# Kernel optimization log

Hardware: AMD Instinct MI355X
Metric: run time of the kernel (lower is better)

The kernel has to match this reference:

```python
import jax, jax.numpy as jnp
import numpy as np

B, S, HID = 4, 8192, 768
H, D, K = 12, 64, 16
KW = 4
TTT_BASE_LR = 1.0
ROPE_THETA = 10000.0
ETA_DECAY_RATE = 0.0
LN_EPS = 1e-5


def setup_inputs() -> dict:
    key = jax.random.key(0)
    ks = jax.random.split(key, 12)
    def randn(k, shape, scale):
        return jax.random.normal(k, shape, jnp.float32) * scale
    def lecun(k, fan_in, shape):
        return jax.random.normal(k, shape, jnp.float32) / np.sqrt(fan_in).astype(np.float32)
    return {
        "x": randn(ks[0], (B, S, HID), 1.0),
        "wq": lecun(ks[1], HID, (HID, H * D)),
        "wv": lecun(ks[2], HID, (HID, H * D)),
        "wo": lecun(ks[3], H * D, (H * D, HID)),  # zeros in source init; randomized for a non-trivial baseline
        "wg": lecun(ks[4], HID, (HID, H * D)),
        "conv_q_w": randn(ks[5], (KW, H * D), 0.1),
        "conv_q_b": jnp.zeros((H * D,), jnp.float32),
        "conv_k_w": randn(ks[6], (KW, H * D), 0.1),
        "conv_k_b": jnp.zeros((H * D,), jnp.float32),
        "lr_w": randn(ks[7], (H, HID), 0.02),
        "lr_b": jnp.zeros((H,), jnp.float32),
        "learnable_token_idx": jnp.zeros((K,), jnp.float32),
        "ttt_norm_scale": jnp.ones((H, 1, D), jnp.float32),
        "ttt_norm_bias": jnp.zeros((H, 1, D), jnp.float32),
        "post_norm_scale": jnp.ones((H * D,), jnp.float32),
        "post_norm_bias": jnp.zeros((H * D,), jnp.float32),
        "W1": randn(ks[8], (H, D, D), 0.02),
        "b1": jnp.zeros((H, 1, D), jnp.float32),
    }


def causal_dwconv(x, w, b):
    # x: [B,S,C], w: [KW,C], b: [C]. Replicates left-pad(KW-1) + flax SAME conv + crop:
    # out[t] = b + sum_k w[k] * x[t + k - KW]  (strictly causal, excludes current token)
    S_ = x.shape[1]
    xp = jnp.pad(x, ((0, 0), (KW, 0), (0, 0)))
    out = b
    for k in range(KW):
        out = out + w[k] * xp[:, k:k + S_]
    return out


def rope(x, cos, sin):
    # x: [B,S,H,D]; interleaved-pair rotation; cos/sin: [S, D//2]
    xr = x.reshape(*x.shape[:-1], D // 2, 2)
    x1, x2 = xr[..., 0], xr[..., 1]
    c = cos[None, :, None, :]
    s = sin[None, :, None, :]
    return jnp.stack([x1 * c - x2 * s, x1 * s + x2 * c], axis=-1).reshape(x.shape)


def ln_fwd(x, g, b):
    mu = x.mean(-1, keepdims=True)
    var = x.var(-1, keepdims=True)
    return (x - mu) * jax.lax.rsqrt(var + LN_EPS) * g + b


def ln_l2_bwd(x, target, g, b):
    # grad of 0.5*||LN(x)*g+b - target||^2 wrt x (fused form)
    mu = x.mean(-1, keepdims=True)
    var = x.var(-1, keepdims=True)
    std = jnp.sqrt(var + LN_EPS)
    xh = (x - mu) / std
    gx = (xh * g + b - target) * g
    return (gx - gx.mean(-1, keepdims=True) - xh * (gx * xh).mean(-1, keepdims=True)) / std


def ttt_forward(x, wq, wv, wo, wg, conv_q_w, conv_q_b, conv_k_w, conv_k_b,
                lr_w, lr_b, learnable_token_idx, ttt_norm_scale, ttt_norm_bias,
                post_norm_scale, post_norm_bias, W1, b1):
    Bx, Sx, _ = x.shape
    n_mb = Sx // K
    xqk = x @ wq
    XQ = causal_dwconv(xqk, conv_q_w, conv_q_b).reshape(Bx, Sx, H, D)
    XK = causal_dwconv(xqk, conv_k_w, conv_k_b).reshape(Bx, Sx, H, D)
    XV = (x @ wv).reshape(Bx, Sx, H, D)

    inv_freq = 1.0 / (ROPE_THETA ** (jnp.arange(0, D, 2, dtype=jnp.float32) / D))
    freqs = jnp.arange(Sx, dtype=jnp.float32)[:, None] * inv_freq[None, :]
    cos, sin = jnp.cos(freqs), jnp.sin(freqs)
    XQ = rope(XQ, cos, sin)
    XK = rope(XK, cos, sin)

    # per-token learning rates
    token_idx = jnp.maximum(1.0 / jnp.arange(1, K + 1, dtype=jnp.float32) + learnable_token_idx, 0.0)  # [K]
    ttt_lr = jax.nn.sigmoid(jnp.einsum('bsd,hd->bhs', x, lr_w) + lr_b[None, :, None])  # [B,H,S]
    ttt_lr_eta = (TTT_BASE_LR / D) * ttt_lr
    decay = jnp.exp(ETA_DECAY_RATE * (jnp.arange(K, dtype=jnp.float32) - (K - 1)))  # [K]
    # eta[b,h,m,i,j] = token_idx[i] * lr[b,h,m,j] * decay[j]
    eta = token_idx[None, None, None, :, None] * (ttt_lr_eta.reshape(Bx, H, n_mb, 1, K) * decay)

    to_mb = lambda t: t.reshape(Bx, n_mb, K, H, D).transpose(1, 0, 3, 2, 4)  # [n_mb,B,H,K,D]
    xs = (to_mb(XQ), to_mb(XK), to_mb(XV), eta.transpose(2, 0, 1, 3, 4))

    W1_0 = jnp.broadcast_to(W1[None], (Bx, H, D, D)) + 0.0
    b1_0 = jnp.broadcast_to(b1[None], (Bx, H, 1, D)) + 0.0
    tril = jnp.tril(jnp.ones((K, K), jnp.float32))

    def step(carry, inp):
        W1c, b1c = carry
        q, k, v, e = inp  # [B,H,K,D], e: [B,H,K,K]
        Z1 = jnp.einsum('bhkd,bhde->bhke', k, W1c) + b1c
        grad = ln_l2_bwd(Z1, v - k, ttt_norm_scale, ttt_norm_bias)  # [B,H,K,D]
        Attn = jnp.einsum('bhid,bhjd->bhij', q, k) * tril
        b1_bar = b1c - jnp.einsum('bhij,bhjd->bhid', e * tril, grad)
        Z1_bar = jnp.einsum('bhkd,bhde->bhke', q, W1c) \
                 - jnp.einsum('bhij,bhjd->bhid', e * Attn, grad) + b1_bar
        last_e = e[..., -1, :, None]  # [B,H,K,1]
        W1n = W1c - jnp.einsum('bhkd,bhke->bhde', last_e * k, grad)
        b1n = b1c - jnp.sum(last_e * grad, axis=-2, keepdims=True)
        out = q + ln_fwd(Z1_bar, ttt_norm_scale, ttt_norm_bias)
        return (W1n, b1n), out

    _, Z = jax.lax.scan(step, (W1_0, b1_0), xs)  # Z: [n_mb,B,H,K,D]
    Z = Z.transpose(1, 0, 3, 2, 4).reshape(Bx, Sx, H * D)

    mu = Z.mean(-1, keepdims=True)
    var = Z.var(-1, keepdims=True)
    Zn = (Z - mu) * jax.lax.rsqrt(var + LN_EPS) * post_norm_scale + post_norm_bias
    gate = jax.nn.gelu(x @ wg)
    return (Zn * gate) @ wo


def reference(x, wq, wv, wo, wg, conv_q_w, conv_q_b, conv_k_w, conv_k_b,
              lr_w, lr_b, learnable_token_idx, ttt_norm_scale, ttt_norm_bias,
              post_norm_scale, post_norm_bias, W1, b1):
    return ttt_forward(x, wq, wv, wo, wg, conv_q_w, conv_q_b, conv_k_w, conv_k_b,
                       lr_w, lr_b, learnable_token_idx, ttt_norm_scale, ttt_norm_bias,
                       post_norm_scale, post_norm_bias, W1, b1)
```

## Files before the change

### kernel.cpp

```cpp
#include <hip/hip_runtime.h>
#include <hip/hip_bf16.h>
#include <math.h>

#define BB 4
#define SSEQ 8192
#define HIDDEN 768
#define NH 12
#define DDIM 64
#define KMB 16
#define NMB 512
#define NTOK ((size_t)BB * SSEQ)
#define NELT (NTOK * HIDDEN)
#define WELT (768 * 768)

typedef short bf16x8 __attribute__((ext_vector_type(8)));
typedef float f32x4 __attribute__((ext_vector_type(4)));

union frag_u {
  bf16x8 v;
  unsigned u32[4];
  unsigned short u16[8];
};

__device__ __forceinline__ f32x4 mfma16(bf16x8 a, bf16x8 b, f32x4 c) {
  return __builtin_amdgcn_mfma_f32_16x16x32_bf16(a, b, c, 0, 0, 0);
}

__device__ __forceinline__ float wave_sum(float v) {
#pragma unroll
  for (int off = 32; off > 0; off >>= 1) v += __shfl_xor(v, off, 64);
  return v;
}

template <int CTRL>
__device__ __forceinline__ float dpp_add(float v) {
  union { float f; int i; } a, b;
  a.f = v;
  b.i = __builtin_amdgcn_update_dpp(0, a.i, CTRL, 0xF, 0xF, true);
  return v + b.f;
}
__device__ __forceinline__ float rsum16(float v) {
  v = dpp_add<0x121>(v);
  v = dpp_add<0x122>(v);
  v = dpp_add<0x124>(v);
  v = dpp_add<0x128>(v);
  return v;
}

__device__ __forceinline__ unsigned short bf16hi(float x) {
  union { float f; unsigned u; } a; a.f = x;
  return (unsigned short)((a.u + 0x8000u) >> 16);
}
__device__ __forceinline__ unsigned pack_bf16(float f0, float f1) {
  union { float f; unsigned u; } a, b; a.f = f0; b.f = f1;
  return __builtin_amdgcn_perm(b.u + 0x8000u, a.u + 0x8000u, 0x07060302u);
}
__device__ __forceinline__ float bf2f(unsigned short s) {
  union { unsigned u; float f; } a; a.u = ((unsigned)s) << 16; return a.f;
}
__device__ __forceinline__ float gelu_tanh(float x) {
  float x3 = x * x * x;
  return 0.5f * x * (1.0f + tanhf(0.7978845608028654f * (x + 0.044715f * x3)));
}

__device__ __forceinline__ void glds16(const void* g, void* l) {
  __builtin_amdgcn_global_load_lds(
      (const __attribute__((address_space(1))) void*)g,
      (__attribute__((address_space(3))) void*)l, 16, 0, 0);
}

__global__ __launch_bounds__(256) void cvt_x_kernel(
    const float* __restrict__ x, unsigned short* __restrict__ xb) {
  const size_t gid = (size_t)blockIdx.x * 256 + threadIdx.x;
  const float4 v = *(const float4*)(x + gid * 4);
  uint2 r; r.x = pack_bf16(v.x, v.y); r.y = pack_bf16(v.z, v.w);
  *(uint2*)(xb + gid * 4) = r;
}

__global__ __launch_bounds__(256) void cvt_wT_kernel(
    const float* __restrict__ W, unsigned short* __restrict__ WT) {
  __shared__ float tile[32][33];
  const int tx = threadIdx.x & 31, ty = threadIdx.x >> 5;
  const int k0 = blockIdx.x * 32, n0 = blockIdx.y * 32;
#pragma unroll
  for (int r = 0; r < 4; ++r)
    tile[ty + 8 * r][tx] = W[(size_t)(k0 + ty + 8 * r) * 768 + n0 + tx];
  __syncthreads();
#pragma unroll
  for (int r = 0; r < 4; ++r)
    WT[(size_t)(n0 + ty + 8 * r) * 768 + k0 + tx] = bf16hi(tile[tx][ty + 8 * r]);
}

__global__ __launch_bounds__(256) void gemm_mfma(
    const unsigned short* __restrict__ A, const unsigned short* __restrict__ BT,
    void* __restrict__ Cout, int mode) {
  __shared__ __align__(16) unsigned short Asl[128 * 32];
  __shared__ __align__(16) unsigned short Bsl[128 * 32];
  const int tid = threadIdx.x;
  const int wave = tid >> 6, lane = tid & 63;
  const int n16 = lane & 15, g16 = lane >> 4;
  const int wm = (wave >> 1) * 64, wn = (wave & 1) * 64;
  const int m0 = blockIdx.x * 128, n0 = blockIdx.y * 128;

  const int srow = tid >> 2;
  const int sseg = (tid & 3) * 8;

  const unsigned short* aSrc0 = A + (size_t)(m0 + srow) * 768 + sseg;
  const unsigned short* aSrc1 = A + (size_t)(m0 + 64 + srow) * 768 + sseg;
  const unsigned short* bSrc0 = BT + (size_t)(n0 + srow) * 768 + sseg;
  const unsigned short* bSrc1 = BT + (size_t)(n0 + 64 + srow) * 768 + sseg;
  char* aDst0 = (char*)Asl + wave * 1024;
  char* aDst1 = (char*)Asl + 4096 + wave * 1024;
  char* bDst0 = (char*)Bsl + wave * 1024;
  char* bDst1 = (char*)Bsl + 4096 + wave * 1024;

  f32x4 acc[4][4];
#pragma unroll
  for (int i = 0; i < 4; ++i)
#pragma unroll
    for (int j = 0; j < 4; ++j) { acc[i][j][0] = 0.f; acc[i][j][1] = 0.f; acc[i][j][2] = 0.f; acc[i][j][3] = 0.f; }

  for (int k0 = 0; k0 < 768; k0 += 32) {
    __syncthreads();
    glds16(aSrc0 + k0, aDst0);
    glds16(aSrc1 + k0, aDst1);
    glds16(bSrc0 + k0, bDst0);
    glds16(bSrc1 + k0, bDst1);
    __syncthreads();
    bf16x8 af[4], bfr[4];
#pragma unroll
    for (int mf = 0; mf < 4; ++mf)
      af[mf] = *(const bf16x8*)(Asl + (wm + mf * 16 + n16) * 32 + g16 * 8);
#pragma unroll
    for (int nf = 0; nf < 4; ++nf)
      bfr[nf] = *(const bf16x8*)(Bsl + (wn + nf * 16 + n16) * 32 + g16 * 8);
#pragma unroll
    for (int mf = 0; mf < 4; ++mf)
#pragma unroll
      for (int nf = 0; nf < 4; ++nf)
        acc[mf][nf] = mfma16(af[mf], bfr[nf], acc[mf][nf]);
  }

  const int erow0 = m0 + wm + 4 * g16;
  const int ecol0 = n0 + wn + n16;
  if (mode == 2) {
    float* C = (float*)Cout;
#pragma unroll
    for (int mf = 0; mf < 4; ++mf)
#pragma unroll
      for (int nf = 0; nf < 4; ++nf)
#pragma unroll
        for (int r = 0; r < 4; ++r)
          C[(size_t)(erow0 + mf * 16 + r) * HIDDEN + ecol0 + nf * 16] = acc[mf][nf][r];
  } else if (mode == 1) {
    unsigned short* C = (unsigned short*)Cout;
#pragma unroll
    for (int mf = 0; mf < 4; ++mf)
#pragma unroll
      for (int nf = 0; nf < 4; ++nf)
#pragma unroll
        for (int r = 0; r < 4; ++r)
          C[(size_t)(erow0 + mf * 16 + r) * HIDDEN + ecol0 + nf * 16] = bf16hi(gelu_tanh(acc[mf][nf][r]));
  } else {
    unsigned short* C = (unsigned short*)Cout;
#pragma unroll
    for (int mf = 0; mf < 4; ++mf)
#pragma unroll
      for (int nf = 0; nf < 4; ++nf)
#pragma unroll
        for (int r = 0; r < 4; ++r)
          C[(size_t)(erow0 + mf * 16 + r) * HIDDEN + ecol0 + nf * 16] = bf16hi(acc[mf][nf][r]);
  }
}

__global__ __launch_bounds__(256) void lrpre_kernel(
    const float* __restrict__ x, const float* __restrict__ lrw,
    const float* __restrict__ lrb, float* __restrict__ lrpre) {
  const int g = threadIdx.x >> 6, l = threadIdx.x & 63;
  const int t = blockIdx.x * 4 + g;
  const float* xr = x + (size_t)t * HIDDEN;
  float xv[12];
#pragma unroll
  for (int j = 0; j < 12; ++j) xv[j] = xr[l + 64 * j];
  const int b = t >> 13, s = t & (SSEQ - 1);
  for (int h = 0; h < NH; ++h) {
    const float* wr = lrw + (size_t)h * HIDDEN;
    float a = 0.f;
#pragma unroll
    for (int j = 0; j < 12; ++j) a += xv[j] * wr[l + 64 * j];
    a = wave_sum(a);
    if (l == 0) lrpre[((size_t)b * NH + h) * SSEQ + s] = a + lrb[h];
  }
}

__global__ __launch_bounds__(256) void convrope_kernel(
    const __hip_bfloat16* __restrict__ xqk,
    const float* __restrict__ cqw, const float* __restrict__ cqb,
    const float* __restrict__ ckw, const float* __restrict__ ckb,
    __hip_bfloat16* __restrict__ XQ, __hip_bfloat16* __restrict__ XK) {
  const size_t gid = (size_t)blockIdx.x * 256 + threadIdx.x;
  const int p = (int)(gid % 384);
  const size_t bt = gid / 384;
  const int t = (int)(bt & (SSEQ - 1));
  const int c0 = 2 * p, c1 = c0 + 1;
  float q0 = cqb[c0], q1 = cqb[c1], k0v = ckb[c0], k1v = ckb[c1];
#pragma unroll
  for (int kk = 0; kk < 4; ++kk) {
    const int tp = t - 4 + kk;
    if (tp >= 0) {
      const size_t src = (bt - t + tp) * HIDDEN;
      const float x0 = __bfloat162float(xqk[src + c0]);
      const float x1 = __bfloat162float(xqk[src + c1]);
      q0  += cqw[kk * HIDDEN + c0] * x0;  q1  += cqw[kk * HIDDEN + c1] * x1;
      k0v += ckw[kk * HIDDEN + c0] * x0;  k1v += ckw[kk * HIDDEN + c1] * x1;
    }
  }
  const int f = p & 31;
  const float invf = expf(-(float)f * 0.28782313662425572f);
  const float ang = (float)t * invf;
  float sn, cs;
  sincosf(ang, &sn, &cs);
  const size_t o = bt * HIDDEN;
  XQ[o + c0] = __float2bfloat16(q0 * cs - q1 * sn);
  XQ[o + c1] = __float2bfloat16(q0 * sn + q1 * cs);
  XK[o + c0] = __float2bfloat16(k0v * cs - k1v * sn);
  XK[o + c1] = __float2bfloat16(k0v * sn + k1v * cs);
}

struct ScanBuf {
  uint2 qa[2][2], ka[2][2], va[2][2];
  float lr[4];
};

__global__ __launch_bounds__(64) void scan_mfma_kernel(
    const __hip_bfloat16* __restrict__ XQg, const __hip_bfloat16* __restrict__ XKg,
    const __hip_bfloat16* __restrict__ XVg, const float* __restrict__ lrpre,
    const float* __restrict__ lti, const float* __restrict__ tnsg,
    const float* __restrict__ tnbg, const float* __restrict__ W1g,
    const float* __restrict__ b1g, __hip_bfloat16* __restrict__ Zg) {
  const int bh = blockIdx.x;
  const int b = bh / NH, h = bh % NH;
  const int lane = threadIdx.x;
  const int n = lane & 15, g16 = lane >> 4;
  const float inv64 = 1.0f / 64.0f;

  const unsigned short* XQb = (const unsigned short*)XQg + (size_t)b * SSEQ * HIDDEN + h * 64;
  const unsigned short* XKb = (const unsigned short*)XKg + (size_t)b * SSEQ * HIDDEN + h * 64;
  const unsigned short* XVb = (const unsigned short*)XVg + (size_t)b * SSEQ * HIDDEN + h * 64;
  unsigned short* Zb = (unsigned short*)Zg + (size_t)b * SSEQ * HIDDEN + h * 64;
  const float* lrp = lrpre + ((size_t)b * NH + h) * SSEQ;

  f32x4 W1acc[4][4];
#pragma unroll
  for (int db = 0; db < 4; ++db)
#pragma unroll
    for (int eb = 0; eb < 4; ++eb)
#pragma unroll
      for (int r = 0; r < 4; ++r)
        W1acc[db][eb][r] = W1g[(size_t)h * 4096 + (16 * db + 4 * g16 + r) * 64 + 16 * eb + n];

  float b1r[4], tnsr[4], tnbr[4];
#pragma unroll
  for (int eb = 0; eb < 4; ++eb) {
    const int e = h * 64 + 16 * eb + n;
    b1r[eb] = b1g[e]; tnsr[eb] = tnsg[e]; tnbr[eb] = tnbg[e];
  }
  const float tok_n = fmaxf(1.0f / (float)(n + 1) + lti[n], 0.0f);
  const float tok15 = __shfl(tok_n, 15, 64);

  frag_u id0, id1;
  {
    const unsigned short onebf = (g16 == (n >> 2)) ? (unsigned short)0x3F80 : (unsigned short)0;
    const unsigned vsh = ((unsigned)onebf) << (16 * (n & 1));
    const unsigned lo = ((n & 2) == 0) ? vsh : 0u;
    const unsigned hi = ((n & 2) != 0) ? vsh : 0u;
    id0.u32[0] = lo; id0.u32[1] = hi; id0.u32[2] = 0; id0.u32[3] = 0;
    id1.u32[0] = 0;  id1.u32[1] = 0;  id1.u32[2] = lo; id1.u32[3] = hi;
  }
  frag_u onesA;
  onesA.u32[0] = 0x3F803F80u; onesA.u32[1] = 0x3F803F80u;
  onesA.u32[2] = 0x3F803F80u; onesA.u32[3] = 0x3F803F80u;

  int offA[2][2], offC[4][4];
#pragma unroll
  for (int c = 0; c < 2; ++c)
#pragma unroll
    for (int jg = 0; jg < 2; ++jg)
      offA[c][jg] = n * HIDDEN + 16 * (2 * c + jg) + 4 * g16;
#pragma unroll
  for (int blk = 0; blk < 4; ++blk)
#pragma unroll
    for (int r = 0; r < 4; ++r)
      offC[blk][r] = (4 * g16 + r) * HIDDEN + 16 * blk + n;

  auto load_mb = [&](ScanBuf& bf, int mb) {
    const size_t sb = (size_t)mb * (KMB * HIDDEN);
#pragma unroll
    for (int c = 0; c < 2; ++c)
#pragma unroll
      for (int jg = 0; jg < 2; ++jg) {
        bf.qa[c][jg] = *(const uint2*)(XQb + sb + offA[c][jg]);
        bf.ka[c][jg] = *(const uint2*)(XKb + sb + offA[c][jg]);
        bf.va[c][jg] = *(const uint2*)(XVb + sb + offA[c][jg]);
      }
    const float4 l4 = *(const float4*)(lrp + mb * KMB + 4 * g16);
    bf.lr[0] = l4.x; bf.lr[1] = l4.y; bf.lr[2] = l4.z; bf.lr[3] = l4.w;
  };

  auto compute_mb = [&](ScanBuf& bf, int mb) {
    const size_t sb = (size_t)mb * (KMB * HIDDEN);
    float etaj[4];
#pragma unroll
    for (int jj = 0; jj < 4; ++jj)
      etaj[jj] = 1.0f / (64.0f * (1.0f + __expf(-bf.lr[jj])));

    frag_u w1f[2][4];
#pragma unroll
    for (int c = 0; c < 2; ++c)
#pragma unroll
      for (int eb = 0; eb < 4; ++eb) {
        w1f[c][eb].u32[0] = pack_bf16(W1acc[2 * c][eb][0], W1acc[2 * c][eb][1]);
        w1f[c][eb].u32[1] = pack_bf16(W1acc[2 * c][eb][2], W1acc[2 * c][eb][3]);
        w1f[c][eb].u32[2] = pack_bf16(W1acc[2 * c + 1][eb][0], W1acc[2 * c + 1][eb][1]);
        w1f[c][eb].u32[3] = pack_bf16(W1acc[2 * c + 1][eb][2], W1acc[2 * c + 1][eb][3]);
      }
    frag_u kaf[2], qaf[2], vaf[2];
#pragma unroll
    for (int c = 0; c < 2; ++c) {
      kaf[c].u32[0] = bf.ka[c][0].x; kaf[c].u32[1] = bf.ka[c][0].y;
      kaf[c].u32[2] = bf.ka[c][1].x; kaf[c].u32[3] = bf.ka[c][1].y;
      qaf[c].u32[0] = bf.qa[c][0].x; qaf[c].u32[1] = bf.qa[c][0].y;
      qaf[c].u32[2] = bf.qa[c][1].x; qaf[c].u32[3] = bf.qa[c][1].y;
      vaf[c].u32[0] = bf.va[c][0].x; vaf[c].u32[1] = bf.va[c][0].y;
      vaf[c].u32[2] = bf.va[c][1].x; vaf[c].u32[3] = bf.va[c][1].y;
    }

    f32x4 z4; z4[0] = 0.f; z4[1] = 0.f; z4[2] = 0.f; z4[3] = 0.f;
    f32x4 qcf[4], kcf[4], vcf[4];
#pragma unroll
    for (int c = 0; c < 2; ++c) {
      qcf[2 * c]     = mfma16(qaf[c].v, id0.v, z4);
      qcf[2 * c + 1] = mfma16(qaf[c].v, id1.v, z4);
      kcf[2 * c]     = mfma16(kaf[c].v, id0.v, z4);
      kcf[2 * c + 1] = mfma16(kaf[c].v, id1.v, z4);
      vcf[2 * c]     = mfma16(vaf[c].v, id0.v, z4);
      vcf[2 * c + 1] = mfma16(vaf[c].v, id1.v, z4);
    }
    frag_u ktf[4];
#pragma unroll
    for (int mk = 0; mk < 4; ++mk) {
      ktf[mk].u32[0] = pack_bf16(kcf[mk][0], kcf[mk][1]);
      ktf[mk].u32[1] = pack_bf16(kcf[mk][2], kcf[mk][3]);
      ktf[mk].u32[2] = 0; ktf[mk].u32[3] = 0;
    }

    f32x4 zk[4], zq[4];
#pragma unroll
    for (int eb = 0; eb < 4; ++eb) {
      f32x4 init; init[0] = b1r[eb]; init[1] = b1r[eb]; init[2] = b1r[eb]; init[3] = b1r[eb];
      zk[eb] = init; zq[eb] = init;
    }
#pragma unroll
    for (int c = 0; c < 2; ++c)
#pragma unroll
      for (int eb = 0; eb < 4; ++eb) {
        zk[eb] = mfma16(kaf[c].v, w1f[c][eb].v, zk[eb]);
        zq[eb] = mfma16(qaf[c].v, w1f[c][eb].v, zq[eb]);
      }
    f32x4 st_; st_[0] = 0.f; st_[1] = 0.f; st_[2] = 0.f; st_[3] = 0.f;
    st_ = mfma16(kaf[0].v, qaf[0].v, st_);
    st_ = mfma16(kaf[1].v, qaf[1].v, st_);

    float s1[4], s2[4];
#pragma unroll
    for (int r = 0; r < 4; ++r) {
      s1[r] = zk[0][r] + zk[1][r] + zk[2][r] + zk[3][r];
      s2[r] = zk[0][r] * zk[0][r] + zk[1][r] * zk[1][r] + zk[2][r] * zk[2][r] + zk[3][r] * zk[3][r];
    }
#pragma unroll
    for (int r = 0; r < 4; ++r) { s1[r] = rsum16(s1[r]); s2[r] = rsum16(s2[r]); }
    float mr[4], rstd[4];
#pragma unroll
    for (int r = 0; r < 4; ++r) {
      mr[r] = s1[r] * inv64;
      rstd[r] = rsqrtf(s2[r] * inv64 - mr[r] * mr[r] + 1e-5f);
    }
    float xh[4][4], gx[4][4], t1[4] = {0.f, 0.f, 0.f, 0.f}, t2[4] = {0.f, 0.f, 0.f, 0.f};
#pragma unroll
    for (int eb = 0; eb < 4; ++eb)
#pragma unroll
      for (int r = 0; r < 4; ++r) {
        const float xh_ = (zk[eb][r] - mr[r]) * rstd[r];
        const float tg = vcf[eb][r] - kcf[eb][r];
        const float gx_ = (xh_ * tnsr[eb] + tnbr[eb] - tg) * tnsr[eb];
        xh[eb][r] = xh_; gx[eb][r] = gx_;
        t1[r] += gx_; t2[r] += gx_ * xh_;
      }
#pragma unroll
    for (int r = 0; r < 4; ++r) { t1[r] = rsum16(t1[r]); t2[r] = rsum16(t2[r]); }
    float g_[4][4];
#pragma unroll
    for (int eb = 0; eb < 4; ++eb)
#pragma unroll
      for (int r = 0; r < 4; ++r)
        g_[eb][r] = (gx[eb][r] - t1[r] * inv64 - xh[eb][r] * (t2[r] * inv64)) * rstd[r];

    frag_u gbf[4];
#pragma unroll
    for (int eb = 0; eb < 4; ++eb) {
      gbf[eb].u32[0] = pack_bf16(g_[eb][0], g_[eb][1]);
      gbf[eb].u32[1] = pack_bf16(g_[eb][2], g_[eb][3]);
      gbf[eb].u32[2] = 0; gbf[eb].u32[3] = 0;
    }
    frag_u coef;
    {
      float cf[4];
#pragma unroll
      for (int jj = 0; jj < 4; ++jj) {
        const int j = 4 * g16 + jj;
        cf[jj] = (j <= n) ? -tok_n * etaj[jj] * (1.0f + st_[jj]) : 0.0f;
      }
      coef.u32[0] = pack_bf16(cf[0], cf[1]);
      coef.u32[1] = pack_bf16(cf[2], cf[3]);
      coef.u32[2] = 0; coef.u32[3] = 0;
    }
    f32x4 zbv[4];
#pragma unroll
    for (int eb = 0; eb < 4; ++eb)
      zbv[eb] = mfma16(coef.v, gbf[eb].v, zq[eb]);

#pragma unroll
    for (int r = 0; r < 4; ++r) {
      s1[r] = zbv[0][r] + zbv[1][r] + zbv[2][r] + zbv[3][r];
      s2[r] = zbv[0][r] * zbv[0][r] + zbv[1][r] * zbv[1][r] + zbv[2][r] * zbv[2][r] + zbv[3][r] * zbv[3][r];
    }
#pragma unroll
    for (int r = 0; r < 4; ++r) { s1[r] = rsum16(s1[r]); s2[r] = rsum16(s2[r]); }
#pragma unroll
    for (int r = 0; r < 4; ++r) {
      mr[r] = s1[r] * inv64;
      rstd[r] = rsqrtf(s2[r] * inv64 - mr[r] * mr[r] + 1e-5f);
    }
#pragma unroll
    for (int eb = 0; eb < 4; ++eb)
#pragma unroll
      for (int r = 0; r < 4; ++r) {
        const float o = qcf[eb][r] + (zbv[eb][r] - mr[r]) * rstd[r] * tnsr[eb] + tnbr[eb];
        Zb[sb + offC[eb][r]] = bf16hi(o);
      }

    float lgv[4][4];
    frag_u lgf[4];
#pragma unroll
    for (int eb = 0; eb < 4; ++eb) {
#pragma unroll
      for (int jj = 0; jj < 4; ++jj) lgv[eb][jj] = -tok15 * etaj[jj] * g_[eb][jj];
      lgf[eb].u32[0] = pack_bf16(lgv[eb][0], lgv[eb][1]);
      lgf[eb].u32[1] = pack_bf16(lgv[eb][2], lgv[eb][3]);
      lgf[eb].u32[2] = 0; lgf[eb].u32[3] = 0;
    }
#pragma unroll
    for (int mk = 0; mk < 4; ++mk)
#pragma unroll
      for (int eb = 0; eb < 4; ++eb)
        W1acc[mk][eb] = mfma16(ktf[mk].v, lgf[eb].v, W1acc[mk][eb]);
#pragma unroll
    for (int eb = 0; eb < 4; ++eb) {
      f32x4 bs = mfma16(onesA.v, lgf[eb].v, z4);
      b1r[eb] += bs[0];
    }
  };

  ScanBuf A, B;
  load_mb(A, 0);
  for (int mb = 0; mb < NMB; mb += 2) {
    load_mb(B, mb + 1);
    compute_mb(A, mb);
    if (mb + 2 < NMB) load_mb(A, mb + 2);
    compute_mb(B, mb + 1);
  }
}

__global__ __launch_bounds__(256) void stats_kernel(
    const __hip_bfloat16* __restrict__ Z, float* __restrict__ st) {
  const int g = threadIdx.x >> 6, l = threadIdx.x & 63;
  const int t = blockIdx.x * 4 + g;
  const __hip_bfloat16* zr = Z + (size_t)t * HIDDEN;
  float zv[12];
  float s_ = 0.f;
#pragma unroll
  for (int j = 0; j < 12; ++j) { zv[j] = __bfloat162float(zr[l + 64 * j]); s_ += zv[j]; }
  s_ = wave_sum(s_);
  const float m = s_ * (1.0f / 768.0f);
  float v_ = 0.f;
#pragma unroll
  for (int j = 0; j < 12; ++j) { const float d = zv[j] - m; v_ += d * d; }
  v_ = wave_sum(v_) * (1.0f / 768.0f);
  if (l == 0) { st[2 * t] = m; st[2 * t + 1] = rsqrtf(v_ + 1e-5f); }
}

__global__ __launch_bounds__(256) void fuse_epi_kernel(
    const unsigned short* __restrict__ Zb, const unsigned short* __restrict__ gateb,
    const float* __restrict__ st, const float* __restrict__ pns,
    const float* __restrict__ pnb, unsigned short* __restrict__ aout) {
  const int gid = blockIdx.x * 256 + threadIdx.x;
  const int t = gid / 192;
  const int c = (gid - t * 192) * 4;
  const float mu = st[2 * t], rstd = st[2 * t + 1];
  const size_t base = (size_t)t * HIDDEN + c;
  const uint2 z2 = *(const uint2*)(Zb + base);
  const uint2 g2 = *(const uint2*)(gateb + base);
  const float4 p4 = *(const float4*)(pns + c);
  const float4 q4 = *(const float4*)(pnb + c);
  const float o0 = ((bf2f((unsigned short)(z2.x & 0xffff)) - mu) * rstd * p4.x + q4.x) * bf2f((unsigned short)(g2.x & 0xffff));
  const float o1 = ((bf2f((unsigned short)(z2.x >> 16)) - mu) * rstd * p4.y + q4.y) * bf2f((unsigned short)(g2.x >> 16));
  const float o2 = ((bf2f((unsigned short)(z2.y & 0xffff)) - mu) * rstd * p4.z + q4.z) * bf2f((unsigned short)(g2.y & 0xffff));
  const float o3 = ((bf2f((unsigned short)(z2.y >> 16)) - mu) * rstd * p4.w + q4.w) * bf2f((unsigned short)(g2.y >> 16));
  uint2 r; r.x = pack_bf16(o0, o1); r.y = pack_bf16(o2, o3);
  *(uint2*)(aout + base) = r;
}

extern "C" void kernel_launch(void* const* d_in, const int* in_sizes, int n_in,
                              void* d_out, int out_size, void* d_ws, size_t ws_size,
                              hipStream_t stream) {
  const float* x   = (const float*)d_in[0];
  const float* wq  = (const float*)d_in[1];
  const float* wv  = (const float*)d_in[2];
  const float* wo  = (const float*)d_in[3];
  const float* wg  = (const float*)d_in[4];
  const float* cqw = (const float*)d_in[5];
  const float* cqb = (const float*)d_in[6];
  const float* ckw = (const float*)d_in[7];
  const float* ckb = (const float*)d_in[8];
  const float* lrw = (const float*)d_in[9];
  const float* lrb = (const float*)d_in[10];
  const float* lti = (const float*)d_in[11];
  const float* tns = (const float*)d_in[12];
  const float* tnb = (const float*)d_in[13];
  const float* pns = (const float*)d_in[14];
  const float* pnb = (const float*)d_in[15];
  const float* W1g = (const float*)d_in[16];
  const float* b1g = (const float*)d_in[17];
  float* out = (float*)d_out;

  unsigned short* zbuf = (unsigned short*)d_ws;
  unsigned short* xqk  = zbuf + NELT;
  unsigned short* xv   = xqk + NELT;
  unsigned short* gate = xv + NELT;
  unsigned short* xq   = gate + NELT;
  unsigned short* xk   = xq + NELT;
  unsigned short* wqT  = xk + NELT;
  unsigned short* wvT  = wqT + WELT;
  unsigned short* wgT  = wvT + WELT;
  unsigned short* woT  = wgT + WELT;
  float* lrpre = (float*)(woT + WELT);
  float* st    = lrpre + (size_t)BB * NH * SSEQ;
  unsigned short* xb   = zbuf;
  unsigned short* aout = xqk;

  const dim3 wtGrid(24, 24);
  cvt_x_kernel<<<(unsigned)(NELT / 4 / 256), 256, 0, stream>>>(x, xb);
  cvt_wT_kernel<<<wtGrid, 256, 0, stream>>>(wq, wqT);
  cvt_wT_kernel<<<wtGrid, 256, 0, stream>>>(wv, wvT);
  cvt_wT_kernel<<<wtGrid, 256, 0, stream>>>(wg, wgT);
  cvt_wT_kernel<<<wtGrid, 256, 0, stream>>>(wo, woT);

  const dim3 gemmGrid((unsigned)(NTOK / 128), HIDDEN / 128);
  gemm_mfma<<<gemmGrid, 256, 0, stream>>>(xb, wqT, (void*)xqk, 0);
  gemm_mfma<<<gemmGrid, 256, 0, stream>>>(xb, wvT, (void*)xv, 0);
  gemm_mfma<<<gemmGrid, 256, 0, stream>>>(xb, wgT, (void*)gate, 1);
  lrpre_kernel<<<(unsigned)(NTOK / 4), 256, 0, stream>>>(x, lrw, lrb, lrpre);
  convrope_kernel<<<(unsigned)(NTOK * 384 / 256), 256, 0, stream>>>(
      (const __hip_bfloat16*)xqk, cqw, cqb, ckw, ckb,
      (__hip_bfloat16*)xq, (__hip_bfloat16*)xk);
  scan_mfma_kernel<<<BB * NH, 64, 0, stream>>>(
      (const __hip_bfloat16*)xq, (const __hip_bfloat16*)xk,
      (const __hip_bfloat16*)xv, lrpre, lti, tns, tnb, W1g, b1g,
      (__hip_bfloat16*)zbuf);
  stats_kernel<<<(unsigned)(NTOK / 4), 256, 0, stream>>>((const __hip_bfloat16*)zbuf, st);
  fuse_epi_kernel<<<(unsigned)(NELT / 4 / 256), 256, 0, stream>>>(zbuf, gate, st, pns, pnb, aout);
  gemm_mfma<<<gemmGrid, 256, 0, stream>>>(aout, woT, (void*)out, 2);
}
```

Before: 1.882 ms.

## Overlap gate GEMM with sequential scan by fusing into one launch

The gate projection GEMM (with GELU) now runs inside the scan launch as extra workgroups. The 48 scan blocks are latency-bound and occupy only a few CUs, so the remaining CUs compute the gate tiles at the same time. Scan waves get raised priority. The buffers are remapped so the scan output goes to the xqk region and the epilogue writes to zbuf. The cost is 192 idle threads per scan block, since 256-thread blocks are launched but only 64 threads scan, and the GEMM variant is simpler, without double buffering.

Result: faster. 1.789 ms (-4.9%).

```diff
diff --git a/kernel.cpp b/kernel.cpp
--- a/kernel.cpp
+++ b/kernel.cpp
@@ -232,12 +232,78 @@
   float lr[4];
 };
 
-__global__ __launch_bounds__(64) void scan_mfma_kernel(
+__global__ __launch_bounds__(256) void fused_scan_gate(
     const __hip_bfloat16* __restrict__ XQg, const __hip_bfloat16* __restrict__ XKg,
     const __hip_bfloat16* __restrict__ XVg, const float* __restrict__ lrpre,
     const float* __restrict__ lti, const float* __restrict__ tnsg,
     const float* __restrict__ tnbg, const float* __restrict__ W1g,
-    const float* __restrict__ b1g, __hip_bfloat16* __restrict__ Zg) {
+    const float* __restrict__ b1g, __hip_bfloat16* __restrict__ Zg,
+    const unsigned short* __restrict__ A, const unsigned short* __restrict__ BT,
+    unsigned short* __restrict__ Cgate) {
+  if (blockIdx.x >= 48) {
+    __shared__ __align__(16) unsigned short Asl[128 * 32];
+    __shared__ __align__(16) unsigned short Bsl[128 * 32];
+    const int bid = blockIdx.x - 48;
+    const int tid = threadIdx.x;
+    const int wave = tid >> 6, lane = tid & 63;
+    const int n16 = lane & 15, g16 = lane >> 4;
+    const int wm = (wave >> 1) * 64, wn = (wave & 1) * 64;
+    const int m0 = (bid & 255) * 128, n0 = (bid >> 8) * 128;
+
+    const int srow = tid >> 2;
+    const int sseg = (tid & 3) * 8;
+
+    const unsigned short* aSrc0 = A + (size_t)(m0 + srow) * 768 + sseg;
+    const unsigned short* aSrc1 = A + (size_t)(m0 + 64 + srow) * 768 + sseg;
+    const unsigned short* bSrc0 = BT + (size_t)(n0 + srow) * 768 + sseg;
+    const unsigned short* bSrc1 = BT + (size_t)(n0 + 64 + srow) * 768 + sseg;
+    char* aDst0 = (char*)Asl + wave * 1024;
+    char* aDst1 = (char*)Asl + 4096 + wave * 1024;
+    char* bDst0 = (char*)Bsl + wave * 1024;
+    char* bDst1 = (char*)Bsl + 4096 + wave * 1024;
+
+    f32x4 acc[4][4];
+#pragma unroll
+    for (int i = 0; i < 4; ++i)
+#pragma unroll
+      for (int j = 0; j < 4; ++j) { acc[i][j][0] = 0.f; acc[i][j][1] = 0.f; acc[i][j][2] = 0.f; acc[i][j][3] = 0.f; }
+
+    for (int k0 = 0; k0 < 768; k0 += 32) {
+      __syncthreads();
+      glds16(aSrc0 + k0, aDst0);
+      glds16(aSrc1 + k0, aDst1);
+      glds16(bSrc0 + k0, bDst0);
+      glds16(bSrc1 + k0, bDst1);
+      __syncthreads();
+      bf16x8 af[4], bfr[4];
+#pragma unroll
+      for (int mf = 0; mf < 4; ++mf)
+        af[mf] = *(const bf16x8*)(Asl + (wm + mf * 16 + n16) * 32 + g16 * 8);
+#pragma unroll
+      for (int nf = 0; nf < 4; ++nf)
+        bfr[nf] = *(const bf16x8*)(Bsl + (wn + nf * 16 + n16) * 32 + g16 * 8);
+#pragma unroll
+      for (int mf = 0; mf < 4; ++mf)
+#pragma unroll
+        for (int nf = 0; nf < 4; ++nf)
+          acc[mf][nf] = mfma16(af[mf], bfr[nf], acc[mf][nf]);
+    }
+
+    const int erow0 = m0 + wm + 4 * g16;
+    const int ecol0 = n0 + wn + n16;
+#pragma unroll
+    for (int mf = 0; mf < 4; ++mf)
+#pragma unroll
+      for (int nf = 0; nf < 4; ++nf)
+#pragma unroll
+        for (int r = 0; r < 4; ++r)
+          Cgate[(size_t)(erow0 + mf * 16 + r) * HIDDEN + ecol0 + nf * 16] = bf16hi(gelu_tanh(acc[mf][nf][r]));
+    return;
+  }
+
+  if (threadIdx.x >= 64) return;
+  __builtin_amdgcn_s_setprio(1);
+
   const int bh = blockIdx.x;
   const int b = bh / NH, h = bh % NH;
   const int lane = threadIdx.x;
@@ -471,14 +537,15 @@
     }
   };
 
-  ScanBuf A, B;
-  load_mb(A, 0);
+  ScanBuf Abuf, Bbuf;
+  load_mb(Abuf, 0);
   for (int mb = 0; mb < NMB; mb += 2) {
-    load_mb(B, mb + 1);
-    compute_mb(A, mb);
-    if (mb + 2 < NMB) load_mb(A, mb + 2);
-    compute_mb(B, mb + 1);
-  }
+    load_mb(Bbuf, mb + 1);
+    compute_mb(Abuf, mb);
+    if (mb + 2 < NMB) load_mb(Abuf, mb + 2);
+    compute_mb(Bbuf, mb + 1);
+  }
+  __builtin_amdgcn_s_setprio(0);
 }
 
 __global__ __launch_bounds__(256) void stats_kernel(
@@ -556,7 +623,8 @@
   float* lrpre = (float*)(woT + WELT);
   float* st    = lrpre + (size_t)BB * NH * SSEQ;
   unsigned short* xb   = zbuf;
-  unsigned short* aout = xqk;
+  unsigned short* zOut = xqk;
+  unsigned short* aout = zbuf;
 
   const dim3 wtGrid(24, 24);
   cvt_x_kernel<<<(unsigned)(NELT / 4 / 256), 256, 0, stream>>>(x, xb);
@@ -568,16 +636,15 @@
   const dim3 gemmGrid((unsigned)(NTOK / 128), HIDDEN / 128);
   gemm_mfma<<<gemmGrid, 256, 0, stream>>>(xb, wqT, (void*)xqk, 0);
   gemm_mfma<<<gemmGrid, 256, 0, stream>>>(xb, wvT, (void*)xv, 0);
-  gemm_mfma<<<gemmGrid, 256, 0, stream>>>(xb, wgT, (void*)gate, 1);
   lrpre_kernel<<<(unsigned)(NTOK / 4), 256, 0, stream>>>(x, lrw, lrb, lrpre);
   convrope_kernel<<<(unsigned)(NTOK * 384 / 256), 256, 0, stream>>>(
       (const __hip_bfloat16*)xqk, cqw, cqb, ckw, ckb,
       (__hip_bfloat16*)xq, (__hip_bfloat16*)xk);
-  scan_mfma_kernel<<<BB * NH, 64, 0, stream>>>(
+  fused_scan_gate<<<48 + 1536, 256, 0, stream>>>(
       (const __hip_bfloat16*)xq, (const __hip_bfloat16*)xk,
       (const __hip_bfloat16*)xv, lrpre, lti, tns, tnb, W1g, b1g,
-      (__hip_bfloat16*)zbuf);
-  stats_kernel<<<(unsigned)(NTOK / 4), 256, 0, stream>>>((const __hip_bfloat16*)zbuf, st);
-  fuse_epi_kernel<<<(unsigned)(NELT / 4 / 256), 256, 0, stream>>>(zbuf, gate, st, pns, pnb, aout);
+      (__hip_bfloat16*)zOut, xb, wgT, gate);
+  stats_kernel<<<(unsigned)(NTOK / 4), 256, 0, stream>>>((const __hip_bfloat16*)zOut, st);
+  fuse_epi_kernel<<<(unsigned)(NELT / 4 / 256), 256, 0, stream>>>(zOut, gate, st, pns, pnb, aout);
   gemm_mfma<<<gemmGrid, 256, 0, stream>>>(aout, woT, (void*)out, 2);
 }
```
